# Performance work log

Hardware: AMD Instinct MI355X
Metric: run time of the kernel (lower is better)

Reference implementation:

```python
import jax, jax.numpy as jnp
import numpy as np

IN_F = 256
OUT_F = 256
ALPHA = 0.2  # leaky-relu slope
NEG_INF = -9e15


def setup_inputs() -> dict:
    key = jax.random.key(0)
    ks = jax.random.split(key, 8)
    N_e, N_kc = 10000, 2000
    exercise_h = jax.random.normal(ks[0], (N_e, IN_F), dtype=jnp.float32)
    kc_h = jax.random.normal(ks[1], (N_kc, IN_F), dtype=jnp.float32)
    adj = jax.random.randint(ks[2], (N_e, N_kc), 0, 2, dtype=jnp.int32)
    # parameters (kaiming-ish scaling)
    W1 = jax.random.normal(ks[3], (IN_F, OUT_F), dtype=jnp.float32) * np.sqrt(2.0 / IN_F)
    E = jax.random.normal(ks[4], (IN_F, OUT_F), dtype=jnp.float32) * np.sqrt(2.0 / IN_F)
    a = jax.random.normal(ks[5], (2 * OUT_F, 1), dtype=jnp.float32) * np.sqrt(2.0 / (2 * OUT_F))
    rd_w = jax.random.normal(ks[6], (OUT_F, 2 * OUT_F), dtype=jnp.float32) * np.sqrt(2.0 / (2 * OUT_F))
    rd_b = jnp.zeros((OUT_F,), dtype=jnp.float32)
    return {"exercise_h": exercise_h, "kc_h": kc_h, "adj": adj,
            "W1": W1, "E": E, "a": a, "rd_w": rd_w, "rd_b": rd_b}


def reference(exercise_h, kc_h, adj, W1, E, a, rd_w, rd_b):
    kc_Wh = kc_h @ W1            # [N_kc, D]
    ex_Wh = exercise_h @ W1      # [N_e, D]
    # a . concat(ex_Wh_i, kc_Wh_j) == a1.ex_Wh_i + a2.kc_Wh_j  (avoids [N_e,N_kc,2D] tensor)
    a1 = a[:OUT_F, 0]
    a2 = a[OUT_F:, 0]
    e = jax.nn.leaky_relu((ex_Wh @ a1)[:, None] + (kc_Wh @ a2)[None, :], negative_slope=ALPHA)  # [N_e, N_kc]
    logits = jnp.where(adj > 0, e, jnp.float32(NEG_INF))
    attention = jax.nn.softmax(logits, axis=1)
    new_kc = attention @ kc_Wh           # [N_e, D]
    ex_Eh = exercise_h @ E               # [N_e, D]
    feat = jnp.concatenate([new_kc, new_kc * ex_Eh], axis=1)  # [N_e, 2D]
    out = feat @ rd_w.T + rd_b
    return jax.nn.elu(out)
```

## Files before the change

kernel.cpp:

```cpp
#include <hip/hip_runtime.h>

#define N_E 10000
#define N_KC 2000
#define ALPHA 0.2f

typedef __attribute__((ext_vector_type(8))) short short8;
typedef __attribute__((ext_vector_type(4))) float f32x4;

__device__ float g_w1a1[256];
__device__ float g_t[2048];
__device__ __align__(16) unsigned short g_W1T_pk[16 * 8 * 512];
__device__ __align__(16) unsigned short g_ET_pk[16 * 8 * 512];
__device__ __align__(16) unsigned short g_rdw_pk[16 * 16 * 512];
__device__ __align__(16) unsigned short g_kcWh_pk[16 * 64 * 512];
__device__ __align__(16) unsigned short g_P_pk[626u * 63 * 512];
__device__ float g_inv[10016];

__device__ __forceinline__ unsigned short f2bf(float f) {
  union { float f; unsigned int u; } v; v.f = f;
  unsigned int r = v.u + 0x7FFFu + ((v.u >> 16) & 1u);
  return (unsigned short)(r >> 16);
}

__device__ __forceinline__ void cvt_store4(float4 v, unsigned short* dst) {
  ushort4 o;
  o.x = f2bf(v.x); o.y = f2bf(v.y); o.z = f2bf(v.z); o.w = f2bf(v.w);
  *reinterpret_cast<ushort4*>(dst) = o;
}

__global__ __launch_bounds__(256) void prep_kernel(
    const float* __restrict__ W1, const float* __restrict__ E,
    const float* __restrict__ a, const float* __restrict__ rd_w) {
  int b = blockIdx.x, tid = threadIdx.x;
  if (b < 32) {
#pragma unroll
    for (int s2 = 0; s2 < 2; ++s2) {
      int sId = b * 512 + tid + s2 * 256;
      int ct = sId >> 10, rem = sId & 1023;
      int kt = rem >> 6, lane = rem & 63;
      int g = lane >> 4, r = lane & 15;
      const float* src = rd_w + (size_t)(ct * 16 + r) * 512 + kt * 32 + g * 8;
      unsigned short* dst = g_rdw_pk + (size_t)sId * 8;
      cvt_store4(*(const float4*)src, dst);
      cvt_store4(*(const float4*)(src + 4), dst + 4);
    }
  } else if (b < 48) {
#pragma unroll
    for (int s2 = 0; s2 < 2; ++s2) {
      int sId = (b - 32) * 512 + tid + s2 * 256;
      int ct = sId >> 9, rem = sId & 511;
      int kt = rem >> 6, lane = rem & 63;
      int g = lane >> 4, r = lane & 15;
      int col = ct * 16 + r, k = kt * 32 + g * 8;
      unsigned short* dst = g_W1T_pk + (size_t)sId * 8;
      ushort4 o0, o1;
      o0.x = f2bf(W1[(k + 0) * 256 + col]); o0.y = f2bf(W1[(k + 1) * 256 + col]);
      o0.z = f2bf(W1[(k + 2) * 256 + col]); o0.w = f2bf(W1[(k + 3) * 256 + col]);
      o1.x = f2bf(W1[(k + 4) * 256 + col]); o1.y = f2bf(W1[(k + 5) * 256 + col]);
      o1.z = f2bf(W1[(k + 6) * 256 + col]); o1.w = f2bf(W1[(k + 7) * 256 + col]);
      *(ushort4*)dst = o0; *(ushort4*)(dst + 4) = o1;
    }
  } else if (b < 64) {
#pragma unroll
    for (int s2 = 0; s2 < 2; ++s2) {
      int sId = (b - 48) * 512 + tid + s2 * 256;
      int ct = sId >> 9, rem = sId & 511;
      int kt = rem >> 6, lane = rem & 63;
      int g = lane >> 4, r = lane & 15;
      int col = ct * 16 + r, k = kt * 32 + g * 8;
      unsigned short* dst = g_ET_pk + (size_t)sId * 8;
      ushort4 o0, o1;
      o0.x = f2bf(E[(k + 0) * 256 + col]); o0.y = f2bf(E[(k + 1) * 256 + col]);
      o0.z = f2bf(E[(k + 2) * 256 + col]); o0.w = f2bf(E[(k + 3) * 256 + col]);
      o1.x = f2bf(E[(k + 4) * 256 + col]); o1.y = f2bf(E[(k + 5) * 256 + col]);
      o1.z = f2bf(E[(k + 6) * 256 + col]); o1.w = f2bf(E[(k + 7) * 256 + col]);
      *(ushort4*)dst = o0; *(ushort4*)(dst + 4) = o1;
    }
  } else if (b == 64) {
    float acc = 0.f;
    for (int q = 0; q < 64; ++q) {
      float4 wv = *(const float4*)(W1 + (size_t)tid * 256 + q * 4);
      float4 a4 = *(const float4*)(a + q * 4);
      acc += wv.x * a4.x + wv.y * a4.y + wv.z * a4.z + wv.w * a4.w;
    }
    g_w1a1[tid] = acc;
  } else {
    for (int idx = tid; idx < 16 * 2 * 512; idx += 256) {
      int ct = idx >> 10, rem = idx & 1023;
      int kt = 62 + (rem >> 9), off = rem & 511;
      g_kcWh_pk[((size_t)ct * 64 + kt) * 512 + off] = 0;
    }
    if (tid < 48) g_t[2000 + tid] = 0.f;
  }
}

__global__ __launch_bounds__(256) void kc_mfma_kernel(
    const float* __restrict__ kc_h, const float* __restrict__ a) {
  __shared__ float tred[4][4][4];
  int tid = threadIdx.x, lane = tid & 63, w = tid >> 6;
  int r = lane & 15, g = lane >> 4;
  int j0 = blockIdx.x * 16;
  f32x4 acc[4] = {{0.f,0.f,0.f,0.f},{0.f,0.f,0.f,0.f},
                  {0.f,0.f,0.f,0.f},{0.f,0.f,0.f,0.f}};
  for (int kk = 0; kk < 8; ++kk) {
    int k = kk * 32 + g * 8;
    const float* src = kc_h + (size_t)(j0 + r) * 256 + k;
    float4 x0 = *(const float4*)src, x1 = *(const float4*)(src + 4);
    short8 af = {(short)f2bf(x0.x), (short)f2bf(x0.y), (short)f2bf(x0.z),
                 (short)f2bf(x0.w), (short)f2bf(x1.x), (short)f2bf(x1.y),
                 (short)f2bf(x1.z), (short)f2bf(x1.w)};
#pragma unroll
    for (int n = 0; n < 4; ++n) {
      short8 bf = *(const short8*)(g_W1T_pk + ((size_t)(w * 4 + n) * 8 + kk) *
                                                  512 + lane * 8);
      acc[n] = __builtin_amdgcn_mfma_f32_16x16x32_bf16(af, bf, acc[n], 0, 0, 0);
    }
  }
  int j = j0 + g * 4;
  int kt = j >> 5, lsub = ((j >> 3) & 3) * 16 + r, sub = (g & 1) * 4;
#pragma unroll
  for (int n = 0; n < 4; ++n) {
    int ct = w * 4 + n;
    ushort4 o;
    o.x = f2bf(acc[n][0]); o.y = f2bf(acc[n][1]);
    o.z = f2bf(acc[n][2]); o.w = f2bf(acc[n][3]);
    *reinterpret_cast<ushort4*>(
        g_kcWh_pk + ((size_t)ct * 64 + kt) * 512 + lsub * 8 + sub) = o;
  }
  float a2v[4];
#pragma unroll
  for (int n = 0; n < 4; ++n) a2v[n] = a[256 + w * 64 + n * 16 + r];
  float tp[4];
#pragma unroll
  for (int q = 0; q < 4; ++q)
    tp[q] = acc[0][q] * a2v[0] + acc[1][q] * a2v[1] + acc[2][q] * a2v[2] +
            acc[3][q] * a2v[3];
#pragma unroll
  for (int off = 1; off < 16; off <<= 1)
#pragma unroll
    for (int q = 0; q < 4; ++q) tp[q] += __shfl_xor(tp[q], off, 64);
  if (r == 0)
#pragma unroll
    for (int q = 0; q < 4; ++q) tred[w][g][q] = tp[q];
  __syncthreads();
  if (tid < 16)
    g_t[j0 + tid] = tred[0][tid >> 2][tid & 3] + tred[1][tid >> 2][tid & 3] +
                    tred[2][tid >> 2][tid & 3] + tred[3][tid >> 2][tid & 3];
}

__global__ __launch_bounds__(256) void p_gen_kernel(
    const float* __restrict__ exh, const int* __restrict__ adj) {
  __shared__ float t_s[2048];
  __shared__ float sv_s[16];
  __shared__ float ds_red[4][16];
  int tid = threadIdx.x, lane = tid & 63, q = tid >> 6;
  int i0 = blockIdx.x * 16;

  ((float4*)t_s)[tid] = ((const float4*)g_t)[tid];
  ((float4*)t_s)[tid + 256] = ((const float4*)g_t)[tid + 256];

  {
    int row = tid >> 4, seg = tid & 15;
    const float* xsrc = exh + (size_t)(i0 + row) * 256 + seg * 16;
    const float* wsrc = g_w1a1 + seg * 16;
    float sp = 0.f;
#pragma unroll
    for (int j = 0; j < 4; ++j) {
      float4 x = *(const float4*)(xsrc + j * 4);
      float4 wv = *(const float4*)(wsrc + j * 4);
      sp += x.x * wv.x + x.y * wv.y + x.z * wv.z + x.w * wv.w;
    }
    sp += __shfl_xor(sp, 1, 64);
    sp += __shfl_xor(sp, 2, 64);
    sp += __shfl_xor(sp, 4, 64);
    sp += __shfl_xor(sp, 8, 64);
    if (seg == 0) sv_s[row] = sp;
  }
  __syncthreads();

  int r = lane & 15, g = lane >> 4;
  float sv = sv_s[r];
  const int* arow = adj + (size_t)(i0 + r) * N_KC;
  unsigned short* pb = g_P_pk + (size_t)blockIdx.x * 63 * 512 + lane * 8;
  float dsum = 0.f;

#pragma unroll
  for (int m = 0; m < 16; ++m) {
    int kk = m * 4 + q;
    if (kk < 63) {
      int c0 = kk * 32 + g * 8;
      int4 a0 = {0, 0, 0, 0}, a1 = {0, 0, 0, 0};
      if (c0 + 8 <= N_KC) {
        a0 = *(const int4*)(arow + c0);
        a1 = *(const int4*)(arow + c0 + 4);
      }
      float4 t0 = *(const float4*)(t_s + c0);
      float4 t1 = *(const float4*)(t_s + c0 + 4);
      float tv[8] = {t0.x, t0.y, t0.z, t0.w, t1.x, t1.y, t1.z, t1.w};
      int av[8] = {a0.x, a0.y, a0.z, a0.w, a1.x, a1.y, a1.z, a1.w};
      unsigned ub[8];
#pragma unroll
      for (int j = 0; j < 8; ++j) {
        float x = sv + tv[j];
        float lx = fmaxf(x, ALPHA * x);
        float pv = (av[j] > 0) ? __expf(lx) : 0.f;
        dsum += pv;
        ub[j] = __float_as_uint(pv) + 0x8000u;
      }
      int4 pk;
      pk.x = (int)((ub[0] >> 16) | (ub[1] & 0xFFFF0000u));
      pk.y = (int)((ub[2] >> 16) | (ub[3] & 0xFFFF0000u));
      pk.z = (int)((ub[4] >> 16) | (ub[5] & 0xFFFF0000u));
      pk.w = (int)((ub[6] >> 16) | (ub[7] & 0xFFFF0000u));
      *(int4*)(pb + (size_t)kk * 512) = pk;
    }
  }

  dsum += __shfl_xor(dsum, 16, 64);
  dsum += __shfl_xor(dsum, 32, 64);
  if (lane < 16) ds_red[q][lane] = dsum;
  __syncthreads();
  if (tid < 16) {
    float s = ds_red[0][tid] + ds_red[1][tid] + ds_red[2][tid] + ds_red[3][tid];
    g_inv[i0 + tid] = 1.f / fmaxf(s, 1e-30f);
  }
}

#define FST 536
__global__ __launch_bounds__(512, 4) void g_gemm_kernel(
    const float* __restrict__ exh, const float* __restrict__ rd_b,
    float* __restrict__ out) {
  __shared__ __align__(16) unsigned char smem[34816];
  __shared__ float inv_s[32];
  unsigned short* exh_pk_s = (unsigned short*)smem;
  unsigned short* feat_s = (unsigned short*)smem;

  int tid = threadIdx.x, w = tid >> 6, lane = tid & 63;
  int r = lane & 15, g = lane >> 4;
  int i0 = blockIdx.x * 32;

  {
#pragma unroll
    for (int m = 0; m < 2; ++m) {
      int row = i0 + m * 16 + r; row = row < N_E ? row : N_E - 1;
      const float* xsrc = exh + (size_t)row * 256 + w * 32 + g * 8;
      float4 x0 = *(const float4*)xsrc, x1 = *(const float4*)(xsrc + 4);
      unsigned short* dst = exh_pk_s + m * 4096 + w * 512 + lane * 8;
      cvt_store4(x0, dst); cvt_store4(x1, dst + 4);
    }
  }
  if (tid < 32) {
    int row = i0 + tid;
    inv_s[tid] = g_inv[row < N_E ? row : 0];
  }

  f32x4 accP[2][2] = {{{0.f,0.f,0.f,0.f},{0.f,0.f,0.f,0.f}},
                      {{0.f,0.f,0.f,0.f},{0.f,0.f,0.f,0.f}}};
  const unsigned short* pa0 =
      g_P_pk + (size_t)(blockIdx.x * 2 + 0) * 63 * 512 + lane * 8;
  const unsigned short* pa1 =
      g_P_pk + (size_t)(blockIdx.x * 2 + 1) * 63 * 512 + lane * 8;
  const unsigned short* bb0 =
      g_kcWh_pk + (size_t)(w * 2 + 0) * 64 * 512 + lane * 8;
  const unsigned short* bb1 =
      g_kcWh_pk + (size_t)(w * 2 + 1) * 64 * 512 + lane * 8;
#pragma unroll 7
  for (int kk = 0; kk < 63; ++kk) {
    short8 a0 = *(const short8*)(pa0 + (size_t)kk * 512);
    short8 a1 = *(const short8*)(pa1 + (size_t)kk * 512);
    short8 b0 = *(const short8*)(bb0 + (size_t)kk * 512);
    short8 b1 = *(const short8*)(bb1 + (size_t)kk * 512);
    accP[0][0] = __builtin_amdgcn_mfma_f32_16x16x32_bf16(a0, b0, accP[0][0], 0, 0, 0);
    accP[1][0] = __builtin_amdgcn_mfma_f32_16x16x32_bf16(a1, b0, accP[1][0], 0, 0, 0);
    accP[0][1] = __builtin_amdgcn_mfma_f32_16x16x32_bf16(a0, b1, accP[0][1], 0, 0, 0);
    accP[1][1] = __builtin_amdgcn_mfma_f32_16x16x32_bf16(a1, b1, accP[1][1], 0, 0, 0);
  }

  __syncthreads();

  f32x4 accE[2][2] = {{{0.f,0.f,0.f,0.f},{0.f,0.f,0.f,0.f}},
                      {{0.f,0.f,0.f,0.f},{0.f,0.f,0.f,0.f}}};
#pragma unroll
  for (int kk = 0; kk < 8; ++kk) {
    short8 a0 = *(const short8*)(exh_pk_s + kk * 512 + lane * 8);
    short8 a1 = *(const short8*)(exh_pk_s + 4096 + kk * 512 + lane * 8);
#pragma unroll
    for (int n = 0; n < 2; ++n) {
      short8 bf = *(const short8*)(g_ET_pk + ((size_t)(w * 2 + n) * 8 + kk) *
                                                 512 + lane * 8);
      accE[0][n] = __builtin_amdgcn_mfma_f32_16x16x32_bf16(a0, bf, accE[0][n], 0, 0, 0);
      accE[1][n] = __builtin_amdgcn_mfma_f32_16x16x32_bf16(a1, bf, accE[1][n], 0, 0, 0);
    }
  }
  __syncthreads();

  int c0e = w * 32;
#pragma unroll
  for (int m = 0; m < 2; ++m)
#pragma unroll
    for (int n = 0; n < 2; ++n) {
      int col = c0e + n * 16 + r;
#pragma unroll
      for (int q2 = 0; q2 < 4; ++q2) {
        int row = m * 16 + g * 4 + q2;
        float nk = accP[m][n][q2] * inv_s[row];
        feat_s[(size_t)row * FST + col] = f2bf(nk);
        feat_s[(size_t)row * FST + 256 + col] = f2bf(nk * accE[m][n][q2]);
      }
    }
  __syncthreads();

  f32x4 accO[2][2] = {{{0.f,0.f,0.f,0.f},{0.f,0.f,0.f,0.f}},
                      {{0.f,0.f,0.f,0.f},{0.f,0.f,0.f,0.f}}};
#pragma unroll
  for (int kt = 0; kt < 16; ++kt) {
    int k = kt * 32 + g * 8;
    short8 a0 = *(const short8*)(feat_s + (size_t)r * FST + k);
    short8 a1 = *(const short8*)(feat_s + (size_t)(16 + r) * FST + k);
#pragma unroll
    for (int n = 0; n < 2; ++n) {
      short8 bf = *(const short8*)(g_rdw_pk + ((size_t)(w * 2 + n) * 16 + kt) *
                                                  512 + lane * 8);
      accO[0][n] = __builtin_amdgcn_mfma_f32_16x16x32_bf16(a0, bf, accO[0][n], 0, 0, 0);
      accO[1][n] = __builtin_amdgcn_mfma_f32_16x16x32_bf16(a1, bf, accO[1][n], 0, 0, 0);
    }
  }
#pragma unroll
  for (int m = 0; m < 2; ++m) {
    if (i0 + m * 16 >= N_E) continue;
#pragma unroll
    for (int n = 0; n < 2; ++n) {
      int col = c0e + n * 16 + r;
      float bias = rd_b[col];
#pragma unroll
      for (int q2 = 0; q2 < 4; ++q2) {
        int row = i0 + m * 16 + g * 4 + q2;
        float x = accO[m][n][q2] + bias;
        float res = x > 0.f ? x : (__expf(x) - 1.f);
        out[(size_t)row * 256 + col] = res;
      }
    }
  }
}

extern "C" void kernel_launch(void* const* d_in, const int* in_sizes, int n_in,
                              void* d_out, int out_size, void* d_ws,
                              size_t ws_size, hipStream_t stream) {
  const float* exh  = (const float*)d_in[0];
  const float* kc_h = (const float*)d_in[1];
  const int*   adj  = (const int*)d_in[2];
  const float* W1   = (const float*)d_in[3];
  const float* E    = (const float*)d_in[4];
  const float* a    = (const float*)d_in[5];
  const float* rd_w = (const float*)d_in[6];
  const float* rd_b = (const float*)d_in[7];
  float* out = (float*)d_out;

  prep_kernel<<<66, 256, 0, stream>>>(W1, E, a, rd_w);
  kc_mfma_kernel<<<N_KC / 16, 256, 0, stream>>>(kc_h, a);
  p_gen_kernel<<<N_E / 16, 256, 0, stream>>>(exh, adj);
  g_gemm_kernel<<<(N_E + 31) / 32, 512, 0, stream>>>(exh, rd_b, out);
}
```

Baseline: 222.6 us.

## Coalesce adjacency reads per row and stage P tile in LDS for GEMM

p_gen_kernel now has each wave process whole adjacency rows with contiguous int4 reads across lanes, reducing each row sum with a wave shuffle. This removes the shared-memory cross-wave reduction and the strided 8-int access pattern. g_gemm_kernel shrinks to 16 rows per block, doubling the grid, and first copies the block's packed P tile into LDS so the MFMA loop reads A from LDS instead of global memory. The cost is 72KB of LDS per block, which under launch_bounds(512,4) may limit occupancy, and half the reuse of kcWh B-fragments per block.

```diff
diff --git a/kernel.cpp b/kernel.cpp
--- a/kernel.cpp
+++ b/kernel.cpp
@@ -152,7 +152,6 @@
     const float* __restrict__ exh, const int* __restrict__ adj) {
   __shared__ float t_s[2048];
   __shared__ float sv_s[16];
-  __shared__ float ds_red[4][16];
   int tid = threadIdx.x, lane = tid & 63, q = tid >> 6;
   int i0 = blockIdx.x * 16;
 
@@ -178,51 +177,46 @@
   }
   __syncthreads();
 
-  int r = lane & 15, g = lane >> 4;
-  float sv = sv_s[r];
-  const int* arow = adj + (size_t)(i0 + r) * N_KC;
-  unsigned short* pb = g_P_pk + (size_t)blockIdx.x * 63 * 512 + lane * 8;
-  float dsum = 0.f;
-
-#pragma unroll
-  for (int m = 0; m < 16; ++m) {
-    int kk = m * 4 + q;
-    if (kk < 63) {
-      int c0 = kk * 32 + g * 8;
-      int4 a0 = {0, 0, 0, 0}, a1 = {0, 0, 0, 0};
-      if (c0 + 8 <= N_KC) {
-        a0 = *(const int4*)(arow + c0);
-        a1 = *(const int4*)(arow + c0 + 4);
+  unsigned short* tbase = g_P_pk + (size_t)blockIdx.x * 63 * 512;
+
+#pragma unroll 2
+  for (int rr = 0; rr < 4; ++rr) {
+    int row = q * 4 + rr;
+    float svr = sv_s[row];
+    const int* arow = adj + (size_t)(i0 + row) * N_KC;
+    float rsum = 0.f;
+#pragma unroll
+    for (int i = 0; i < 8; ++i) {
+      int c0 = i * 256 + lane * 4;
+      int4 av = {0, 0, 0, 0};
+      if (c0 + 4 <= N_KC) av = *(const int4*)(arow + c0);
+      float4 tv = *(const float4*)(t_s + c0);
+      float xs[4] = {svr + tv.x, svr + tv.y, svr + tv.z, svr + tv.w};
+      int as[4] = {av.x, av.y, av.z, av.w};
+      float pv[4];
+#pragma unroll
+      for (int j = 0; j < 4; ++j) {
+        float lx = fmaxf(xs[j], ALPHA * xs[j]);
+        pv[j] = (as[j] > 0) ? __expf(lx) : 0.f;
+        rsum += pv[j];
       }
-      float4 t0 = *(const float4*)(t_s + c0);
-      float4 t1 = *(const float4*)(t_s + c0 + 4);
-      float tv[8] = {t0.x, t0.y, t0.z, t0.w, t1.x, t1.y, t1.z, t1.w};
-      int av[8] = {a0.x, a0.y, a0.z, a0.w, a1.x, a1.y, a1.z, a1.w};
-      unsigned ub[8];
-#pragma unroll
-      for (int j = 0; j < 8; ++j) {
-        float x = sv + tv[j];
-        float lx = fmaxf(x, ALPHA * x);
-        float pv = (av[j] > 0) ? __expf(lx) : 0.f;
-        dsum += pv;
-        ub[j] = __float_as_uint(pv) + 0x8000u;
+      if (c0 < 2016) {
+        unsigned u0 = ((__float_as_uint(pv[0]) + 0x8000u) >> 16) |
+                      ((__float_as_uint(pv[1]) + 0x8000u) & 0xFFFF0000u);
+        unsigned u1 = ((__float_as_uint(pv[2]) + 0x8000u) >> 16) |
+                      ((__float_as_uint(pv[3]) + 0x8000u) & 0xFFFF0000u);
+        int kk = c0 >> 5, g2 = (c0 >> 3) & 3, h = (c0 >> 2) & 1;
+        uint2 st; st.x = u0; st.y = u1;
+        *(uint2*)(tbase + (size_t)kk * 512 + (row + 16 * g2) * 8 + 4 * h) = st;
       }
-      int4 pk;
-      pk.x = (int)((ub[0] >> 16) | (ub[1] & 0xFFFF0000u));
-      pk.y = (int)((ub[2] >> 16) | (ub[3] & 0xFFFF0000u));
-      pk.z = (int)((ub[4] >> 16) | (ub[5] & 0xFFFF0000u));
-      pk.w = (int)((ub[6] >> 16) | (ub[7] & 0xFFFF0000u));
-      *(int4*)(pb + (size_t)kk * 512) = pk;
-    }
-  }
-
-  dsum += __shfl_xor(dsum, 16, 64);
-  dsum += __shfl_xor(dsum, 32, 64);
-  if (lane < 16) ds_red[q][lane] = dsum;
-  __syncthreads();
-  if (tid < 16) {
-    float s = ds_red[0][tid] + ds_red[1][tid] + ds_red[2][tid] + ds_red[3][tid];
-    g_inv[i0 + tid] = 1.f / fmaxf(s, 1e-30f);
+    }
+    rsum += __shfl_xor(rsum, 1, 64);
+    rsum += __shfl_xor(rsum, 2, 64);
+    rsum += __shfl_xor(rsum, 4, 64);
+    rsum += __shfl_xor(rsum, 8, 64);
+    rsum += __shfl_xor(rsum, 16, 64);
+    rsum += __shfl_xor(rsum, 32, 64);
+    if (lane == 0) g_inv[i0 + row] = 1.f / fmaxf(rsum, 1e-30f);
   }
 }
 
@@ -230,115 +224,96 @@
 __global__ __launch_bounds__(512, 4) void g_gemm_kernel(
     const float* __restrict__ exh, const float* __restrict__ rd_b,
     float* __restrict__ out) {
-  __shared__ __align__(16) unsigned char smem[34816];
-  __shared__ float inv_s[32];
-  unsigned short* exh_pk_s = (unsigned short*)smem;
+  __shared__ __align__(16) unsigned char smem[73728];
+  __shared__ float inv_s[16];
+  unsigned short* A_lds = (unsigned short*)smem;
+  unsigned short* exh_pk_s = (unsigned short*)(smem + 65536);
   unsigned short* feat_s = (unsigned short*)smem;
 
   int tid = threadIdx.x, w = tid >> 6, lane = tid & 63;
   int r = lane & 15, g = lane >> 4;
-  int i0 = blockIdx.x * 32;
+  int i0 = blockIdx.x * 16;
 
   {
-#pragma unroll
-    for (int m = 0; m < 2; ++m) {
-      int row = i0 + m * 16 + r; row = row < N_E ? row : N_E - 1;
-      const float* xsrc = exh + (size_t)row * 256 + w * 32 + g * 8;
-      float4 x0 = *(const float4*)xsrc, x1 = *(const float4*)(xsrc + 4);
-      unsigned short* dst = exh_pk_s + m * 4096 + w * 512 + lane * 8;
-      cvt_store4(x0, dst); cvt_store4(x1, dst + 4);
-    }
-  }
-  if (tid < 32) {
-    int row = i0 + tid;
-    inv_s[tid] = g_inv[row < N_E ? row : 0];
-  }
-
-  f32x4 accP[2][2] = {{{0.f,0.f,0.f,0.f},{0.f,0.f,0.f,0.f}},
-                      {{0.f,0.f,0.f,0.f},{0.f,0.f,0.f,0.f}}};
-  const unsigned short* pa0 =
-      g_P_pk + (size_t)(blockIdx.x * 2 + 0) * 63 * 512 + lane * 8;
-  const unsigned short* pa1 =
-      g_P_pk + (size_t)(blockIdx.x * 2 + 1) * 63 * 512 + lane * 8;
+    const int4* srcA = (const int4*)(g_P_pk + (size_t)blockIdx.x * 63 * 512);
+    int4* dstA = (int4*)A_lds;
+#pragma unroll
+    for (int rnd = 0; rnd < 8; ++rnd) {
+      int idx = rnd * 512 + tid;
+      if (idx < 4032) dstA[idx] = srcA[idx];
+    }
+  }
+  {
+    const float* xsrc = exh + (size_t)(i0 + r) * 256 + w * 32 + g * 8;
+    float4 x0 = *(const float4*)xsrc, x1 = *(const float4*)(xsrc + 4);
+    unsigned short* dst = exh_pk_s + w * 512 + lane * 8;
+    cvt_store4(x0, dst); cvt_store4(x1, dst + 4);
+  }
+  if (tid < 16) inv_s[tid] = g_inv[i0 + tid];
+  __syncthreads();
+
+  f32x4 accP[2] = {{0.f,0.f,0.f,0.f},{0.f,0.f,0.f,0.f}};
   const unsigned short* bb0 =
       g_kcWh_pk + (size_t)(w * 2 + 0) * 64 * 512 + lane * 8;
   const unsigned short* bb1 =
       g_kcWh_pk + (size_t)(w * 2 + 1) * 64 * 512 + lane * 8;
 #pragma unroll 7
   for (int kk = 0; kk < 63; ++kk) {
-    short8 a0 = *(const short8*)(pa0 + (size_t)kk * 512);
-    short8 a1 = *(const short8*)(pa1 + (size_t)kk * 512);
+    short8 a  = *(const short8*)(A_lds + (size_t)kk * 512 + lane * 8);
     short8 b0 = *(const short8*)(bb0 + (size_t)kk * 512);
     short8 b1 = *(const short8*)(bb1 + (size_t)kk * 512);
-    accP[0][0] = __builtin_amdgcn_mfma_f32_16x16x32_bf16(a0, b0, accP[0][0], 0, 0, 0);
-    accP[1][0] = __builtin_amdgcn_mfma_f32_16x16x32_bf16(a1, b0, accP[1][0], 0, 0, 0);
-    accP[0][1] = __builtin_amdgcn_mfma_f32_16x16x32_bf16(a0, b1, accP[0][1], 0, 0, 0);
-    accP[1][1] = __builtin_amdgcn_mfma_f32_16x16x32_bf16(a1, b1, accP[1][1], 0, 0, 0);
-  }
-
-  __syncthreads();
-
-  f32x4 accE[2][2] = {{{0.f,0.f,0.f,0.f},{0.f,0.f,0.f,0.f}},
-                      {{0.f,0.f,0.f,0.f},{0.f,0.f,0.f,0.f}}};
+    accP[0] = __builtin_amdgcn_mfma_f32_16x16x32_bf16(a, b0, accP[0], 0, 0, 0);
+    accP[1] = __builtin_amdgcn_mfma_f32_16x16x32_bf16(a, b1, accP[1], 0, 0, 0);
+  }
+
+  f32x4 accE[2] = {{0.f,0.f,0.f,0.f},{0.f,0.f,0.f,0.f}};
 #pragma unroll
   for (int kk = 0; kk < 8; ++kk) {
     short8 a0 = *(const short8*)(exh_pk_s + kk * 512 + lane * 8);
-    short8 a1 = *(const short8*)(exh_pk_s + 4096 + kk * 512 + lane * 8);
 #pragma unroll
     for (int n = 0; n < 2; ++n) {
       short8 bf = *(const short8*)(g_ET_pk + ((size_t)(w * 2 + n) * 8 + kk) *
                                                  512 + lane * 8);
-      accE[0][n] = __builtin_amdgcn_mfma_f32_16x16x32_bf16(a0, bf, accE[0][n], 0, 0, 0);
-      accE[1][n] = __builtin_amdgcn_mfma_f32_16x16x32_bf16(a1, bf, accE[1][n], 0, 0, 0);
-    }
-  }
-  __syncthreads();
-
-  int c0e = w * 32;
-#pragma unroll
-  for (int m = 0; m < 2; ++m)
-#pragma unroll
-    for (int n = 0; n < 2; ++n) {
-      int col = c0e + n * 16 + r;
-#pragma unroll
-      for (int q2 = 0; q2 < 4; ++q2) {
-        int row = m * 16 + g * 4 + q2;
-        float nk = accP[m][n][q2] * inv_s[row];
-        feat_s[(size_t)row * FST + col] = f2bf(nk);
-        feat_s[(size_t)row * FST + 256 + col] = f2bf(nk * accE[m][n][q2]);
-      }
-    }
-  __syncthreads();
-
-  f32x4 accO[2][2] = {{{0.f,0.f,0.f,0.f},{0.f,0.f,0.f,0.f}},
-                      {{0.f,0.f,0.f,0.f},{0.f,0.f,0.f,0.f}}};
+      accE[n] = __builtin_amdgcn_mfma_f32_16x16x32_bf16(a0, bf, accE[n], 0, 0, 0);
+    }
+  }
+  __syncthreads();
+
+#pragma unroll
+  for (int n = 0; n < 2; ++n) {
+    int col = w * 32 + n * 16 + r;
+#pragma unroll
+    for (int q2 = 0; q2 < 4; ++q2) {
+      int row = g * 4 + q2;
+      float nk = accP[n][q2] * inv_s[row];
+      feat_s[(size_t)row * FST + col] = f2bf(nk);
+      feat_s[(size_t)row * FST + 256 + col] = f2bf(nk * accE[n][q2]);
+    }
+  }
+  __syncthreads();
+
+  f32x4 accO[2] = {{0.f,0.f,0.f,0.f},{0.f,0.f,0.f,0.f}};
 #pragma unroll
   for (int kt = 0; kt < 16; ++kt) {
     int k = kt * 32 + g * 8;
     short8 a0 = *(const short8*)(feat_s + (size_t)r * FST + k);
-    short8 a1 = *(const short8*)(feat_s + (size_t)(16 + r) * FST + k);
 #pragma unroll
     for (int n = 0; n < 2; ++n) {
       short8 bf = *(const short8*)(g_rdw_pk + ((size_t)(w * 2 + n) * 16 + kt) *
                                                   512 + lane * 8);
-      accO[0][n] = __builtin_amdgcn_mfma_f32_16x16x32_bf16(a0, bf, accO[0][n], 0, 0, 0);
-      accO[1][n] = __builtin_amdgcn_mfma_f32_16x16x32_bf16(a1, bf, accO[1][n], 0, 0, 0);
-    }
-  }
-#pragma unroll
-  for (int m = 0; m < 2; ++m) {
-    if (i0 + m * 16 >= N_E) continue;
-#pragma unroll
-    for (int n = 0; n < 2; ++n) {
-      int col = c0e + n * 16 + r;
-      float bias = rd_b[col];
-#pragma unroll
-      for (int q2 = 0; q2 < 4; ++q2) {
-        int row = i0 + m * 16 + g * 4 + q2;
-        float x = accO[m][n][q2] + bias;
-        float res = x > 0.f ? x : (__expf(x) - 1.f);
-        out[(size_t)row * 256 + col] = res;
-      }
+      accO[n] = __builtin_amdgcn_mfma_f32_16x16x32_bf16(a0, bf, accO[n], 0, 0, 0);
+    }
+  }
+#pragma unroll
+  for (int n = 0; n < 2; ++n) {
+    int col = w * 32 + n * 16 + r;
+    float bias = rd_b[col];
+#pragma unroll
+    for (int q2 = 0; q2 < 4; ++q2) {
+      int row = i0 + g * 4 + q2;
+      float x = accO[n][q2] + bias;
+      float res = x > 0.f ? x : (__expf(x) - 1.f);
+      out[(size_t)row * 256 + col] = res;
     }
   }
 }
@@ -359,5 +334,5 @@
   prep_kernel<<<66, 256, 0, stream>>>(W1, E, a, rd_w);
   kc_mfma_kernel<<<N_KC / 16, 256, 0, stream>>>(kc_h, a);
   p_gen_kernel<<<N_E / 16, 256, 0, stream>>>(exh, adj);
-  g_gemm_kernel<<<(N_E + 31) / 32, 512, 0, stream>>>(exh, rd_b, out);
-}
+  g_gemm_kernel<<<N_E / 16, 512, 0, stream>>>(exh, rd_b, out);
+}
```

After: 255.1 us. +14.6%, slower.
